# Optimization experiments

Measured on AMD Instinct MI355X. Metric: run time of the kernel, lower is better.

## Reference

```python
import jax, jax.numpy as jnp
import numpy as np

B, ND, NS, V, D, H, N, NL = 1024, 13, 26, 10000, 64, 8, 16, 4
SEQ = 1 + ND + NS  # cls + dense fields + sparse fields = 40


def _ln(x, g, b):
    m = x.mean(-1, keepdims=True)
    v = x.var(-1, keepdims=True)
    return (x - m) / jnp.sqrt(v + 1e-5) * g + b


def _mamba(x, g, b, xW, xb, A, Dp, oW, ob):
    # Faithful to MambaBlock: normed x feeds proj, state, and D-skip; residual is pre-norm x.
    xn = _ln(x, g, b)
    xp = xn @ xW.T + xb                              # (B,L,2D)
    delta, Bm = jnp.split(xp, 2, axis=-1)
    delta = jax.nn.softplus(delta)
    # h in torch is (B,L,D,1); (h*A_disc).sum(-1) == h * sum_n exp(delta*A[:,n])
    gate = jnp.exp(delta[..., None] * A).sum(-1)     # (B,L,D)
    h = jnp.cumsum(xn * Bm, axis=1)                  # (B,L,D)
    out = h * gate + xn * Dp
    return out @ oW.T + ob + x


def _fwd(dense_x, dense_W, dense_b, embed_tables, cls_token, mb_norm_g, mb_norm_b, mb_xproj_W, mb_xproj_b, mb_A, mb_D, mb_out_W, mb_out_b, merge_W, merge_b, attn_in_W, attn_in_b, attn_out_W, attn_out_b, mlp_W1, mlp_b1, mlp_W2, mlp_b2, mlp_W3, mlp_b3, sparse_idx):
    Bsz = dense_x.shape[0]
    dense_emb = (dense_x @ dense_W.T + dense_b).reshape(Bsz, ND, D)
    idx = jnp.clip(sparse_idx, 0, V)                 # clamp(0, num_embeddings-1)
    sparse_emb = embed_tables[jnp.arange(NS)[None, :], idx]   # (B,NS,D)
    seq = jnp.concatenate([jnp.broadcast_to(cls_token, (Bsz, 1, D)), dense_emb, sparse_emb], axis=1)
    for i in range(NL):
        f = _mamba(seq, mb_norm_g[i, 0], mb_norm_b[i, 0], mb_xproj_W[i, 0], mb_xproj_b[i, 0], mb_A[i, 0], mb_D[i, 0], mb_out_W[i, 0], mb_out_b[i, 0])
        r = _mamba(seq[:, ::-1], mb_norm_g[i, 1], mb_norm_b[i, 1], mb_xproj_W[i, 1], mb_xproj_b[i, 1], mb_A[i, 1], mb_D[i, 1], mb_out_W[i, 1], mb_out_b[i, 1])[:, ::-1]
        seq = jnp.concatenate([f, r], axis=-1) @ merge_W[i].T + merge_b[i]
    # nn.MultiheadAttention (batch_first, eval): packed qkv proj, scaled dot-product, out proj
    qkv = seq @ attn_in_W.T + attn_in_b
    q, k, v = jnp.split(qkv, 3, axis=-1)
    hd = D // H
    rs = lambda t: t.reshape(Bsz, SEQ, H, hd).transpose(0, 2, 1, 3)
    q, k, v = rs(q), rs(k), rs(v)
    att = jax.nn.softmax(jnp.einsum('bhqd,bhkd->bhqk', q, k) / float(np.sqrt(hd)), axis=-1)
    ao = jnp.einsum('bhqk,bhkd->bhqd', att, v).transpose(0, 2, 1, 3).reshape(Bsz, SEQ, D)
    seq = seq + ao @ attn_out_W.T + attn_out_b
    c = seq[:, 0]
    h1 = jax.nn.relu(c @ mlp_W1.T + mlp_b1)
    h2 = jax.nn.relu(h1 @ mlp_W2.T + mlp_b2)
    return (h2 @ mlp_W3.T + mlp_b3)[:, 0]


def setup_inputs():
    ks = iter(jax.random.split(jax.random.key(0), 64))
    nrm = lambda shape, s=0.02: jax.random.normal(next(ks), shape, jnp.float32) * s
    inp = {}
    inp['dense_x'] = jax.random.normal(next(ks), (B, ND), jnp.float32)
    inp['dense_W'] = nrm((ND * D, ND)); inp['dense_b'] = jnp.zeros((ND * D,), jnp.float32)
    tbl = nrm((NS, V + 1, D)); inp['embed_tables'] = tbl.at[:, 0, :].set(0.0)  # padding_idx=0
    inp['cls_token'] = nrm((1, 1, D))
    inp['mb_norm_g'] = jnp.ones((NL, 2, D), jnp.float32); inp['mb_norm_b'] = jnp.zeros((NL, 2, D), jnp.float32)
    inp['mb_xproj_W'] = nrm((NL, 2, 2 * D, D)); inp['mb_xproj_b'] = jnp.zeros((NL, 2, 2 * D), jnp.float32)
    inp['mb_A'] = jax.random.uniform(next(ks), (NL, 2, D, N), jnp.float32, -0.01, 0.01)
    inp['mb_D'] = jnp.ones((NL, 2, D), jnp.float32)
    inp['mb_out_W'] = nrm((NL, 2, D, D)); inp['mb_out_b'] = jnp.zeros((NL, 2, D), jnp.float32)
    inp['merge_W'] = nrm((NL, D, 2 * D)); inp['merge_b'] = jnp.zeros((NL, D), jnp.float32)
    inp['attn_in_W'] = nrm((3 * D, D)); inp['attn_in_b'] = jnp.zeros((3 * D,), jnp.float32)
    inp['attn_out_W'] = nrm((D, D)); inp['attn_out_b'] = jnp.zeros((D,), jnp.float32)
    inp['mlp_W1'] = nrm((128, D)); inp['mlp_b1'] = jnp.zeros((128,), jnp.float32)
    inp['mlp_W2'] = nrm((64, 128)); inp['mlp_b2'] = jnp.zeros((64,), jnp.float32)
    inp['mlp_W3'] = nrm((1, 64)); inp['mlp_b3'] = jnp.zeros((1,), jnp.float32)
    inp['sparse_x'] = jax.random.randint(next(ks), (B, NS), 0, V, jnp.int32)
    return inp


def reference(dense_x, dense_W, dense_b, embed_tables, cls_token, mb_norm_g, mb_norm_b, mb_xproj_W, mb_xproj_b, mb_A, mb_D, mb_out_W, mb_out_b, merge_W, merge_b, attn_in_W, attn_in_b, attn_out_W, attn_out_b, mlp_W1, mlp_b1, mlp_W2, mlp_b2, mlp_W3, mlp_b3, sparse_x):
    return _fwd(dense_x, dense_W, dense_b, embed_tables, cls_token, mb_norm_g, mb_norm_b, mb_xproj_W, mb_xproj_b, mb_A, mb_D, mb_out_W, mb_out_b, merge_W, merge_b, attn_in_W, attn_in_b, attn_out_W, attn_out_b, mlp_W1, mlp_b1, mlp_W2, mlp_b2, mlp_W3, mlp_b3, sparse_x)
```

## Files before the change

kernel.cpp:

```cpp
#include <hip/hip_runtime.h>

#define DEV static __device__ __forceinline__

typedef __attribute__((ext_vector_type(8))) short bf16x8;
typedef __attribute__((ext_vector_type(4))) float f32x4;

#define MFMA(a, b, c) __builtin_amdgcn_mfma_f32_16x16x32_bf16(a, b, c, 0, 0, 0)

DEV float bf2f(unsigned short h) { return __uint_as_float(((unsigned)h) << 16); }
DEV unsigned short f2bf(float f) {
  unsigned u = __float_as_uint(f);
  u += 0x7fffu + ((u >> 16) & 1u);
  return (unsigned short)(u >> 16);
}
DEV bf16x8 ld8(const unsigned short* p) { return *(const bf16x8*)p; }

DEV float dotg64(const float* x, const float* wrow) {
  const float4* wp = (const float4*)wrow;
  float a0 = 0.f, a1 = 0.f;
  #pragma unroll
  for (int c = 0; c < 8; ++c) {
    float4 u = wp[2*c], v = wp[2*c + 1];
    a0 = fmaf(u.x, x[8*c+0], a0); a0 = fmaf(u.y, x[8*c+1], a0);
    a0 = fmaf(u.z, x[8*c+2], a0); a0 = fmaf(u.w, x[8*c+3], a0);
    a1 = fmaf(v.x, x[8*c+4], a1); a1 = fmaf(v.y, x[8*c+5], a1);
    a1 = fmaf(v.z, x[8*c+6], a1); a1 = fmaf(v.w, x[8*c+7], a1);
  }
  return a0 + a1;
}
DEV float wred64(float v) {
  #pragma unroll
  for (int o = 32; o > 0; o >>= 1) v += __shfl_xor(v, o, 64);
  return v;
}

#define XW_HI 0
#define XW_LO 65536
#define OW_HI 131072
#define OW_LO 163840
#define MW_HI 196608
#define MW_LO 229376
#define AI_HI 262144
#define AI_LO 274432
#define SC_OFF 286720


__global__ void prep_kernel(const float* __restrict__ xW, const float* __restrict__ oW,
                            const float* __restrict__ mW, const float* __restrict__ aiW,
                            const float* __restrict__ Ap, unsigned short* __restrict__ wsb) {
  const int gid = blockIdx.x * blockDim.x + threadIdx.x;
  const int stride = gridDim.x * blockDim.x;
  for (int i = gid; i < 65536; i += stride) {
    float x = xW[i]; unsigned short h = f2bf(x);
    wsb[XW_HI + i] = h; wsb[XW_LO + i] = f2bf(x - bf2f(h));
  }
  for (int i = gid; i < 32768; i += stride) {
    float x = oW[i]; unsigned short h = f2bf(x);
    wsb[OW_HI + i] = h; wsb[OW_LO + i] = f2bf(x - bf2f(h));
  }
  for (int i = gid; i < 32768; i += stride) {
    float x = mW[i]; unsigned short h = f2bf(x);
    wsb[MW_HI + i] = h; wsb[MW_LO + i] = f2bf(x - bf2f(h));
  }
  for (int i = gid; i < 12288; i += stride) {
    float x = aiW[i]; unsigned short h = f2bf(x);
    wsb[AI_HI + i] = h; wsb[AI_LO + i] = f2bf(x - bf2f(h));
  }
  float* sc = (float*)(wsb + SC_OFF);
  for (int i = gid; i < 512; i += stride) {
    int pi = i >> 6, d = i & 63;
    const float* a = Ap + (size_t)i * 16;
    float s1 = 0, s2 = 0, s3 = 0, s4 = 0;
    #pragma unroll
    for (int n = 0; n < 16; ++n) {
      float z = a[n]; float z2 = z * z;
      s1 += z; s2 += z2; s3 += z2 * z; s4 += z2 * z2;
    }
    sc[pi*256 + d]       = s1;
    sc[pi*256 + 64 + d]  = s2 * 0.5f;
    sc[pi*256 + 128 + d] = s3 * (1.f/6.f);
    sc[pi*256 + 192 + d] = s4 * (1.f/24.f);
  }
}

__global__ __launch_bounds__(512, 2)
void Mamba4CTRV9_kernel(
    const float* __restrict__ dense_x, const float* __restrict__ dense_W,
    const float* __restrict__ dense_b, const float* __restrict__ tbl,
    const float* __restrict__ cls, const float* __restrict__ ng,
    const float* __restrict__ nb, const float* __restrict__ xb,
    const float* __restrict__ Dp, const float* __restrict__ ob,
    const float* __restrict__ mb, const float* __restrict__ aib,
    const float* __restrict__ aoW, const float* __restrict__ aob,
    const float* __restrict__ w1, const float* __restrict__ b1,
    const float* __restrict__ w2, const float* __restrict__ b2,
    const float* __restrict__ w3, const float* __restrict__ b3,
    const int* __restrict__ sidx, const unsigned short* __restrict__ wsb,
    float* __restrict__ out) {
  __shared__ __align__(16) unsigned char smem[145408];
  float*          s_seq  = (float*)smem;
  unsigned short* s_xnb  = (unsigned short*)(smem + 40960);
  unsigned short* bG0    = (unsigned short*)(smem + 61440);
  unsigned short* bG1    = (unsigned short*)(smem + 81920);
  unsigned short* bB0    = (unsigned short*)(smem + 102400);
  unsigned short* bB1    = (unsigned short*)(smem + 122880);
  float*          s_small= (float*)(smem + 143360);
  float* g0f = (float*)bG0;
  float* g1f = (float*)bG1;
  const float* scf = (const float*)(wsb + SC_OFF);

  const int tid = threadIdx.x, b = blockIdx.x;
  const int lane = tid & 63, wv = tid >> 6;
  const int arow = lane & 15;
  const int aq = (lane >> 4) * 8;
  const int rq = (lane >> 4) * 4;
  const int rq7 = rq & 7;
  const int swA = (arow & 7) << 3;
  const int aqs0 = aq ^ swA, aqs1 = (aq + 32) ^ swA;

  {
    float* s_dx = s_small;
    int* s_idx = (int*)(s_small + 64);
    if (tid < 64) {
      int br = tid >> 4, k = tid & 15;
      if (k < 13) s_dx[tid] = dense_x[(b*4 + br)*13 + k];
    }
    if (tid >= 64 && tid < 168) {
      int s = tid - 64, br = s / 26, si = s - br*26;
      int v = sidx[(b*4 + br)*26 + si];
      v = v < 0 ? 0 : (v > 10000 ? 10000 : v);
      s_idx[s] = v;
    }
    __syncthreads();
    if (tid < 256) s_seq[(tid >> 6)*40*64 + (tid & 63)] = cls[tid & 63];
    {
      const int br = tid >> 7, j0 = tid & 127;
      float x[13];
      #pragma unroll
      for (int k = 0; k < 13; ++k) x[k] = s_dx[br*16 + k];
      for (int j = j0; j < 832; j += 128) {
        float acc = dense_b[j];
        #pragma unroll
        for (int k = 0; k < 13; ++k) acc = fmaf(x[k], dense_W[j*13 + k], acc);
        s_seq[(br*40 + 1 + (j >> 6))*64 + (j & 63)] = acc;
      }
    }
    for (int e = tid; e < 1664; e += 512) {
      int br = e / 416, rem = e - br*416, s = rem >> 4, c = rem & 15;
      const float4* row = (const float4*)(tbl + ((size_t)(s*10001 + s_idx[br*26 + s]))*64);
      ((float4*)&s_seq[(br*40 + 14 + s)*64])[c] = row[c];
    }
  }
  __syncthreads();

  for (int L = 0; L < 4; ++L) {
    const int pi0 = 2*L, pi1 = 2*L + 1;

    {
      const int half = lane >> 5, dl = lane & 31;
      const float ng0 = ng[pi0*64 + dl], ng1 = ng[pi0*64 + dl + 32];
      const float nb0 = nb[pi0*64 + dl], nb1 = nb[pi0*64 + dl + 32];
      #pragma unroll 1
      for (int it = 0; it < 10; ++it) {
        int t = wv*20 + it*2 + half;
        int e = t*64 + dl;
        float x0 = s_seq[e], x1 = s_seq[e + 32];
        float s = x0 + x1, q = fmaf(x0, x0, x1*x1);
        #pragma unroll
        for (int o = 16; o > 0; o >>= 1) { s += __shfl_xor(s, o, 64); q += __shfl_xor(q, o, 64); }
        float mean = s * (1.f/64.f);
        float var = q * (1.f/64.f) - mean*mean;
        float rs = rsqrtf(var + 1e-5f);
        float xn0 = fmaf((x0 - mean) * rs, ng0, nb0);
        float xn1 = fmaf((x1 - mean) * rs, ng1, nb1);
        int sw = (t & 7) << 3;
        int eb = t << 6;
        s_xnb[eb + (dl ^ sw)] = f2bf(xn0);
        s_xnb[eb + ((dl + 32) ^ sw)] = f2bf(xn1);
      }
    }
    __syncthreads();

    {
      const int j = wv*16 + arow;
      const unsigned short* Wh0 = wsb + XW_HI + pi0*8192 + j*64;
      const unsigned short* Wl0 = wsb + XW_LO + pi0*8192 + j*64;
      const unsigned short* Wh1 = wsb + XW_HI + pi1*8192 + j*64;
      const unsigned short* Wl1 = wsb + XW_LO + pi1*8192 + j*64;
      bf16x8 bh00 = ld8(Wh0 + aq), bh01 = ld8(Wh0 + 32 + aq);
      bf16x8 bl00 = ld8(Wl0 + aq), bl01 = ld8(Wl0 + 32 + aq);
      bf16x8 bh10 = ld8(Wh1 + aq), bh11 = ld8(Wh1 + 32 + aq);
      bf16x8 bl10 = ld8(Wl1 + aq), bl11 = ld8(Wl1 + 32 + aq);
      const float bj0 = xb[pi0*128 + j], bj1 = xb[pi1*128 + j];
      const bool isDelta = (wv < 4);
      float c10=0,c20=0,c30=0,c40=0,c11=0,c21=0,c31=0,c41=0;
      if (isDelta) {
        c10=scf[pi0*256+j]; c20=scf[pi0*256+64+j]; c30=scf[pi0*256+128+j]; c40=scf[pi0*256+192+j];
        c11=scf[pi1*256+j]; c21=scf[pi1*256+64+j]; c31=scf[pi1*256+128+j]; c41=scf[pi1*256+192+j];
      }
      #pragma unroll 1
      for (int mt = 0; mt < 10; ++mt) {
        const unsigned short* A = s_xnb + ((mt*16 + arow) << 6);
        bf16x8 ah0 = ld8(A + aqs0), ah1 = ld8(A + aqs1);
        f32x4 a0 = {0,0,0,0}, a1 = {0,0,0,0};
        a0 = MFMA(ah0, bh00, a0); a0 = MFMA(ah0, bl00, a0);
        a0 = MFMA(ah1, bh01, a0); a0 = MFMA(ah1, bl01, a0);
        a1 = MFMA(ah0, bh10, a1); a1 = MFMA(ah0, bl10, a1);
        a1 = MFMA(ah1, bh11, a1); a1 = MFMA(ah1, bl11, a1);
        const int rbase = mt*16 + rq;
        #pragma unroll
        for (int r = 0; r < 4; ++r) {
          int row = rbase + r;
          int swr = (rq7 + r) << 3;
          float x0v = a0[r] + bj0, x1v = a1[r] + bj1;
          if (isDelta) {
            float sp0 = fmaxf(x0v, 0.f) + __logf(1.f + __expf(-fabsf(x0v)));
            float sp1 = fmaxf(x1v, 0.f) + __logf(1.f + __expf(-fabsf(x1v)));
            int o = (row << 6) + (j ^ swr);
            bG0[o] = f2bf(sp0 * fmaf(sp0, fmaf(sp0, fmaf(sp0, c40, c30), c20), c10));
            bG1[o] = f2bf(sp1 * fmaf(sp1, fmaf(sp1, fmaf(sp1, c41, c31), c21), c11));
          } else {
            int o = (row << 6) + ((j - 64) ^ swr);
            bB0[o] = f2bf(x0v);
            bB1[o] = f2bf(x1v);
          }
        }
      }
    }
    __syncthreads();

    {
      const int d = tid & 63, dir = (tid >> 6) & 1, br = tid >> 7;
      const unsigned short* bmb = dir ? bB1 : bB0;
      unsigned short* gb = dir ? bG1 : bG0;
      const float dpd = Dp[(pi0 + dir)*64 + d];
      const int base = br*40;
      float run = 0.f;
      #pragma unroll
      for (int k = 0; k < 40; ++k) {
        int t = base + (dir ? (39 - k) : k);
        int o = (t << 6) + (d ^ ((t & 7) << 3));
        float xn = bf2f(s_xnb[o]);
        run = fmaf(xn, bf2f(bmb[o]), run);
        float gate = 16.f + bf2f(gb[o]);
        gb[o] = f2bf(fmaf(run, gate, xn * dpd));
      }
    }
    __syncthreads();

    {
      const int j = (wv & 3)*16 + arow;
      const int mt0 = (wv < 4) ? 0 : 5, mt1 = (wv < 4) ? 5 : 10;
      const unsigned short* Wh0 = wsb + OW_HI + pi0*4096 + j*64;
      const unsigned short* Wl0 = wsb + OW_LO + pi0*4096 + j*64;
      const unsigned short* Wh1 = wsb + OW_HI + pi1*4096 + j*64;
      const unsigned short* Wl1 = wsb + OW_LO + pi1*4096 + j*64;
      bf16x8 bh00 = ld8(Wh0 + aq), bh01 = ld8(Wh0 + 32 + aq);
      bf16x8 bl00 = ld8(Wl0 + aq), bl01 = ld8(Wl0 + 32 + aq);
      bf16x8 bh10 = ld8(Wh1 + aq), bh11 = ld8(Wh1 + 32 + aq);
      bf16x8 bl10 = ld8(Wl1 + aq), bl11 = ld8(Wl1 + 32 + aq);
      const float bo0 = ob[pi0*64 + j], bo1 = ob[pi1*64 + j];
      #pragma unroll 1
      for (int mt = mt0; mt < mt1; ++mt) {
        const unsigned short* A0 = bG0 + ((mt*16 + arow) << 6);
        const unsigned short* A1 = bG1 + ((mt*16 + arow) << 6);
        bf16x8 a00 = ld8(A0 + aqs0), a01 = ld8(A0 + aqs1);
        bf16x8 a10 = ld8(A1 + aqs0), a11 = ld8(A1 + aqs1);
        f32x4 c0 = {0,0,0,0}, c1 = {0,0,0,0};
        c0 = MFMA(a00, bh00, c0); c0 = MFMA(a00, bl00, c0);
        c0 = MFMA(a01, bh01, c0); c0 = MFMA(a01, bl01, c0);
        c1 = MFMA(a10, bh10, c1); c1 = MFMA(a10, bl10, c1);
        c1 = MFMA(a11, bh11, c1); c1 = MFMA(a11, bl11, c1);
        const int rbase = mt*16 + rq;
        #pragma unroll
        for (int r = 0; r < 4; ++r) {
          int row = rbase + r;
          int o = (row << 6) + (j ^ ((rq7 + r) << 3));
          float res = s_seq[row*64 + j];
          bB0[o] = f2bf(c0[r] + bo0 + res);
          bB1[o] = f2bf(c1[r] + bo1 + res);
        }
      }
    }
    __syncthreads();

    {
      const int n0 = (wv & 3)*16 + arow;
      const int mt0 = (wv < 4) ? 0 : 5, mt1 = (wv < 4) ? 5 : 10;
      const unsigned short* Wh = wsb + MW_HI + L*8192 + n0*128;
      const unsigned short* Wl = wsb + MW_LO + L*8192 + n0*128;
      bf16x8 bh[4], bl[4];
      #pragma unroll
      for (int ks = 0; ks < 4; ++ks) { bh[ks] = ld8(Wh + ks*32 + aq); bl[ks] = ld8(Wl + ks*32 + aq); }
      const float bo = mb[L*64 + n0];
      #pragma unroll 1
      for (int mt = mt0; mt < mt1; ++mt) {
        const unsigned short* Af = bB0 + ((mt*16 + arow) << 6);
        const unsigned short* Ar = bB1 + ((mt*16 + arow) << 6);
        bf16x8 fh0 = ld8(Af + aqs0), fh1 = ld8(Af + aqs1);
        bf16x8 rh0 = ld8(Ar + aqs0), rh1 = ld8(Ar + aqs1);
        f32x4 a0 = {0,0,0,0};
        a0 = MFMA(fh0, bh[0], a0); a0 = MFMA(fh0, bl[0], a0);
        a0 = MFMA(fh1, bh[1], a0); a0 = MFMA(fh1, bl[1], a0);
        a0 = MFMA(rh0, bh[2], a0); a0 = MFMA(rh0, bl[2], a0);
        a0 = MFMA(rh1, bh[3], a0); a0 = MFMA(rh1, bl[3], a0);
        const int rbase = mt*16 + rq;
        #pragma unroll
        for (int r = 0; r < 4; ++r) {
          int row = rbase + r;
          float v = a0[r] + bo;
          s_seq[row*64 + n0] = v;
          if (L == 3) s_xnb[(row << 6) + (n0 ^ ((rq7 + r) << 3))] = f2bf(v);
        }
      }
    }
    __syncthreads();
  }

  {
    #pragma unroll 1
    for (int i = 0; i < 12; ++i) {
      const int u = wv + 8*i;
      int j, mtk;
      if (u < 80) { j = 64 + (u & 7)*16 + arow; mtk = u >> 3; }
      else {
        int qi = u - 80;
        j = (qi & 3)*16 + arow;
        int p = qi >> 2;
        mtk = p*2 + (p >> 1);
      }
      const unsigned short* Wh = wsb + AI_HI + j*64;
      const unsigned short* Wl = wsb + AI_LO + j*64;
      bf16x8 bh0 = ld8(Wh + aq), bh1 = ld8(Wh + 32 + aq);
      bf16x8 bl0 = ld8(Wl + aq), bl1 = ld8(Wl + 32 + aq);
      const float bj = aib[j];
      const unsigned short* A = s_xnb + ((mtk*16 + arow) << 6);
      bf16x8 ah0 = ld8(A + aqs0), ah1 = ld8(A + aqs1);
      f32x4 a0 = {0,0,0,0};
      a0 = MFMA(ah0, bh0, a0); a0 = MFMA(ah0, bl0, a0);
      a0 = MFMA(ah1, bh1, a0); a0 = MFMA(ah1, bl1, a0);
      const int rbase = mtk*16 + rq;
      #pragma unroll
      for (int r = 0; r < 4; ++r) {
        int row = rbase + r;
        int swr = (rq7 + r) << 3;
        float val = a0[r] + bj;
        if (u < 80) {
          if (j < 128) bB0[(row << 6) + ((j - 64) ^ swr)] = f2bf(val);
          else         bB1[(row << 6) + ((j - 128) ^ swr)] = f2bf(val);
        } else {
          if (row % 40 == 0) g0f[(row/40)*720 + 320 + j] = val;
        }
      }
    }
    if (tid < 256) g0f[(tid >> 6)*720 + 384 + (tid & 63)] = s_seq[(tid >> 6)*40*64 + (tid & 63)];
  }
  __syncthreads();

  for (int e = tid; e < 1280; e += 512) {
    int br = e / 320, rem = e - br*320;
    int h = rem / 40, kk = rem - h*40;
    int row = br*40 + kk;
    int kbase = (row << 6) + ((h*8) ^ ((kk & 7) << 3));
    float acc = 0.f;
    #pragma unroll
    for (int i = 0; i < 8; ++i)
      acc += g0f[br*720 + 320 + h*8 + i] * bf2f(bB0[kbase + i]);
    g0f[br*720 + rem] = acc * 0.35355339059327373f;
  }
  __syncthreads();

  {
    const int hh = wv*4 + (lane >> 4), jl = lane & 15;
    float* pr = g0f + (hh >> 3)*720 + (hh & 7)*40;
    float a = pr[jl];
    float bv = pr[16 + jl];
    float cv = (jl < 8) ? pr[32 + jl] : -1e30f;
    float m = fmaxf(fmaxf(a, bv), cv);
    #pragma unroll
    for (int o = 8; o > 0; o >>= 1) m = fmaxf(m, __shfl_xor(m, o, 16));
    float pa = __expf(a - m), pb = __expf(bv - m), pc = (jl < 8) ? __expf(cv - m) : 0.f;
    float s = pa + pb + pc;
    #pragma unroll
    for (int o = 8; o > 0; o >>= 1) s += __shfl_xor(s, o, 16);
    float inv = 1.f / s;
    pr[jl] = pa * inv;
    pr[16 + jl] = pb * inv;
    if (jl < 8) pr[32 + jl] = pc * inv;
  }
  __syncthreads();

  for (int e = tid; e < 1024; e += 512) {
    const int d = e & 63, qrt = (e >> 6) & 3, br = e >> 8, hh = d >> 3;
    float acc = 0.f;
    #pragma unroll
    for (int k = qrt*10; k < qrt*10 + 10; ++k) {
      int o = ((br*40 + k) << 6) + (d ^ ((k & 7) << 3));
      acc += g0f[br*720 + hh*40 + k] * bf2f(bB1[o]);
    }
    g1f[br*512 + qrt*64 + d] = acc;
  }
  __syncthreads();
  if (tid < 256) {
    float* p = g1f + (tid >> 6)*512;
    int d = tid & 63;
    p[256 + d] = p[d] + p[64 + d] + p[128 + d] + p[192 + d];
  }
  __syncthreads();

  if (tid < 256) {
    int br = tid >> 6, o = tid & 63;
    g0f[br*720 + 448 + o] = g0f[br*720 + 384 + o] + aob[o]
                          + dotg64(&g1f[br*512 + 256], aoW + (size_t)o*64);
  }
  __syncthreads();

  {
    int br = tid >> 7, o = tid & 127;
    g1f[br*512 + 320 + o] = fmaxf(b1[o] + dotg64(&g0f[br*720 + 448], w1 + (size_t)o*64), 0.f);
  }
  __syncthreads();

  if (tid < 256) {
    int br = tid >> 6, o = tid & 63;
    float acc = dotg64(&g1f[br*512 + 320], w2 + (size_t)o*128)
              + dotg64(&g1f[br*512 + 384], w2 + (size_t)o*128 + 64);
    g1f[br*512 + 448 + o] = fmaxf(acc + b2[o], 0.f);
  }
  __syncthreads();

  if (tid < 256) {
    int br = tid >> 6;
    float v = g1f[br*512 + 448 + lane] * w3[lane];
    v = wred64(v);
    if (lane == 0) out[b*4 + br] = v + b3[0];
  }
}

extern "C" void kernel_launch(void* const* d_in, const int* in_sizes, int n_in,
                              void* d_out, int out_size, void* d_ws, size_t ws_size,
                              hipStream_t stream) {
  (void)n_in; (void)ws_size; (void)out_size;
  const float* dense_x = (const float*)d_in[0];
  const float* dense_W = (const float*)d_in[1];
  const float* dense_b = (const float*)d_in[2];
  const float* tbl     = (const float*)d_in[3];
  const float* cls     = (const float*)d_in[4];
  const float* ng      = (const float*)d_in[5];
  const float* nb      = (const float*)d_in[6];
  const float* xW      = (const float*)d_in[7];
  const float* xb      = (const float*)d_in[8];
  const float* Ap      = (const float*)d_in[9];
  const float* Dp      = (const float*)d_in[10];
  const float* oW      = (const float*)d_in[11];
  const float* ob      = (const float*)d_in[12];
  const float* mW      = (const float*)d_in[13];
  const float* mb      = (const float*)d_in[14];
  const float* aiW     = (const float*)d_in[15];
  const float* aib     = (const float*)d_in[16];
  const float* aoW     = (const float*)d_in[17];
  const float* aob     = (const float*)d_in[18];
  const float* w1      = (const float*)d_in[19];
  const float* b1      = (const float*)d_in[20];
  const float* w2      = (const float*)d_in[21];
  const float* b2      = (const float*)d_in[22];
  const float* w3      = (const float*)d_in[23];
  const float* b3      = (const float*)d_in[24];
  const int*   sidx    = (const int*)d_in[25];
  float* out = (float*)d_out;
  unsigned short* wsb = (unsigned short*)d_ws;

  hipLaunchKernelGGL(prep_kernel, dim3(256), dim3(256), 0, stream,
                     xW, oW, mW, aiW, Ap, wsb);

  const int B = in_sizes[0] / 13;
  hipLaunchKernelGGL(Mamba4CTRV9_kernel, dim3(B/4), dim3(512), 0, stream,
                     dense_x, dense_W, dense_b, tbl, cls, ng, nb, xb, Dp, ob, mb,
                     aib, aoW, aob, w1, b1, w2, b2, w3, b3, sidx, wsb, out);
}
```

Before: 251.4 us.

## Fold Mamba out-projection into merge projection via precomputed combined weights

The per-layer out-projection and merge GEMMs are algebraically combined. The prep kernel precomputes merge_W·out_W for each direction, the summed residual weight, and a fused bias. The main kernel then runs one GEMM stage over the two gated outputs plus the residual, which removes one stage, one barrier and one bf16 round-trip through shared memory per layer. The scan loop also stages the residual into bf16 for this purpose. In exchange the prep kernel does more work, and the product weights and bf16-quantized residual may shift numerics slightly.

```diff
diff --git a/kernel.cpp b/kernel.cpp
--- a/kernel.cpp
+++ b/kernel.cpp
@@ -36,17 +36,16 @@
 
 #define XW_HI 0
 #define XW_LO 65536
-#define OW_HI 131072
-#define OW_LO 163840
-#define MW_HI 196608
-#define MW_LO 229376
+#define CW 131072
 #define AI_HI 262144
 #define AI_LO 274432
 #define SC_OFF 286720
+#define BP_OFF 290816
 
 
 __global__ void prep_kernel(const float* __restrict__ xW, const float* __restrict__ oW,
-                            const float* __restrict__ mW, const float* __restrict__ aiW,
+                            const float* __restrict__ ob, const float* __restrict__ mW,
+                            const float* __restrict__ mb, const float* __restrict__ aiW,
                             const float* __restrict__ Ap, unsigned short* __restrict__ wsb) {
   const int gid = blockIdx.x * blockDim.x + threadIdx.x;
   const int stride = gridDim.x * blockDim.x;
@@ -55,12 +54,38 @@
     wsb[XW_HI + i] = h; wsb[XW_LO + i] = f2bf(x - bf2f(h));
   }
   for (int i = gid; i < 32768; i += stride) {
-    float x = oW[i]; unsigned short h = f2bf(x);
-    wsb[OW_HI + i] = h; wsb[OW_LO + i] = f2bf(x - bf2f(h));
-  }
-  for (int i = gid; i < 32768; i += stride) {
-    float x = mW[i]; unsigned short h = f2bf(x);
-    wsb[MW_HI + i] = h; wsb[MW_LO + i] = f2bf(x - bf2f(h));
+    int L = i >> 13, rem = i & 8191;
+    int dir = rem >> 12, n = (rem >> 6) & 63, d = rem & 63;
+    const float* mrow = mW + L*8192 + n*128 + dir*64;
+    const float* ocol = oW + L*8192 + dir*4096 + d;
+    float acc = 0.f;
+    #pragma unroll 8
+    for (int j = 0; j < 64; ++j) acc = fmaf(mrow[j], ocol[j*64], acc);
+    unsigned short h = f2bf(acc);
+    int base = CW + L*24576 + dir*8192;
+    wsb[base + n*64 + d] = h;
+    wsb[base + 4096 + n*64 + d] = f2bf(acc - bf2f(h));
+  }
+  for (int i = gid; i < 16384; i += stride) {
+    int L = i >> 12, n = (i >> 6) & 63, j = i & 63;
+    float v = mW[L*8192 + n*128 + j] + mW[L*8192 + n*128 + 64 + j];
+    unsigned short h = f2bf(v);
+    int base = CW + L*24576 + 16384;
+    wsb[base + n*64 + j] = h;
+    wsb[base + 4096 + n*64 + j] = f2bf(v - bf2f(h));
+  }
+  {
+    float* bp = (float*)(wsb + BP_OFF);
+    for (int i = gid; i < 256; i += stride) {
+      int L = i >> 6, n = i & 63;
+      const float* mrow = mW + L*8192 + n*128;
+      float acc = mb[L*64 + n];
+      #pragma unroll 8
+      for (int j = 0; j < 64; ++j) acc = fmaf(ob[(2*L)*64 + j], mrow[j], acc);
+      #pragma unroll 8
+      for (int j = 0; j < 64; ++j) acc = fmaf(ob[(2*L+1)*64 + j], mrow[64 + j], acc);
+      bp[i] = acc;
+    }
   }
   for (int i = gid; i < 12288; i += stride) {
     float x = aiW[i]; unsigned short h = f2bf(x);
@@ -84,7 +109,7 @@
 }
 
 __global__ __launch_bounds__(512, 2)
-void Mamba4CTRV9_kernel(
+void Mamba4CTRV12_kernel(
     const float* __restrict__ dense_x, const float* __restrict__ dense_W,
     const float* __restrict__ dense_b, const float* __restrict__ tbl,
     const float* __restrict__ cls, const float* __restrict__ ng,
@@ -108,6 +133,7 @@
   float* g0f = (float*)bG0;
   float* g1f = (float*)bG1;
   const float* scf = (const float*)(wsb + SC_OFF);
+  const float* bpf = (const float*)(wsb + BP_OFF);
 
   const int tid = threadIdx.x, b = blockIdx.x;
   const int lane = tid & 63, wv = tid >> 6;
@@ -231,7 +257,7 @@
 
     {
       const int d = tid & 63, dir = (tid >> 6) & 1, br = tid >> 7;
-      const unsigned short* bmb = dir ? bB1 : bB0;
+      unsigned short* bmb = dir ? bB1 : bB0;
       unsigned short* gb = dir ? bG1 : bG0;
       const float dpd = Dp[(pi0 + dir)*64 + d];
       const int base = br*40;
@@ -244,71 +270,48 @@
         run = fmaf(xn, bf2f(bmb[o]), run);
         float gate = 16.f + bf2f(gb[o]);
         gb[o] = f2bf(fmaf(run, gate, xn * dpd));
+        if (dir == 0) bmb[o] = f2bf(s_seq[t*64 + d]);
       }
     }
     __syncthreads();
 
     {
-      const int j = (wv & 3)*16 + arow;
+      const int n0 = (wv & 3)*16 + arow;
       const int mt0 = (wv < 4) ? 0 : 5, mt1 = (wv < 4) ? 5 : 10;
-      const unsigned short* Wh0 = wsb + OW_HI + pi0*4096 + j*64;
-      const unsigned short* Wl0 = wsb + OW_LO + pi0*4096 + j*64;
-      const unsigned short* Wh1 = wsb + OW_HI + pi1*4096 + j*64;
-      const unsigned short* Wl1 = wsb + OW_LO + pi1*4096 + j*64;
-      bf16x8 bh00 = ld8(Wh0 + aq), bh01 = ld8(Wh0 + 32 + aq);
-      bf16x8 bl00 = ld8(Wl0 + aq), bl01 = ld8(Wl0 + 32 + aq);
-      bf16x8 bh10 = ld8(Wh1 + aq), bh11 = ld8(Wh1 + 32 + aq);
-      bf16x8 bl10 = ld8(Wl1 + aq), bl11 = ld8(Wl1 + 32 + aq);
-      const float bo0 = ob[pi0*64 + j], bo1 = ob[pi1*64 + j];
+      const unsigned short* cbase = wsb + CW + L*24576;
+      const unsigned short* C0H = cbase + n0*64;
+      const unsigned short* C0L = cbase + 4096 + n0*64;
+      const unsigned short* C1H = cbase + 8192 + n0*64;
+      const unsigned short* C1L = cbase + 12288 + n0*64;
+      const unsigned short* SH  = cbase + 16384 + n0*64;
+      const unsigned short* SL  = cbase + 20480 + n0*64;
+      bf16x8 c0h0 = ld8(C0H + aq), c0h1 = ld8(C0H + 32 + aq);
+      bf16x8 c0l0 = ld8(C0L + aq), c0l1 = ld8(C0L + 32 + aq);
+      bf16x8 c1h0 = ld8(C1H + aq), c1h1 = ld8(C1H + 32 + aq);
+      bf16x8 c1l0 = ld8(C1L + aq), c1l1 = ld8(C1L + 32 + aq);
+      bf16x8 sh0 = ld8(SH + aq), sh1 = ld8(SH + 32 + aq);
+      bf16x8 sl0 = ld8(SL + aq), sl1 = ld8(SL + 32 + aq);
+      const float bom = bpf[L*64 + n0];
       #pragma unroll 1
       for (int mt = mt0; mt < mt1; ++mt) {
         const unsigned short* A0 = bG0 + ((mt*16 + arow) << 6);
         const unsigned short* A1 = bG1 + ((mt*16 + arow) << 6);
-        bf16x8 a00 = ld8(A0 + aqs0), a01 = ld8(A0 + aqs1);
-        bf16x8 a10 = ld8(A1 + aqs0), a11 = ld8(A1 + aqs1);
-        f32x4 c0 = {0,0,0,0}, c1 = {0,0,0,0};
-        c0 = MFMA(a00, bh00, c0); c0 = MFMA(a00, bl00, c0);
-        c0 = MFMA(a01, bh01, c0); c0 = MFMA(a01, bl01, c0);
-        c1 = MFMA(a10, bh10, c1); c1 = MFMA(a10, bl10, c1);
-        c1 = MFMA(a11, bh11, c1); c1 = MFMA(a11, bl11, c1);
+        const unsigned short* AR = bB0 + ((mt*16 + arow) << 6);
+        bf16x8 g00 = ld8(A0 + aqs0), g01 = ld8(A0 + aqs1);
+        bf16x8 g10 = ld8(A1 + aqs0), g11 = ld8(A1 + aqs1);
+        bf16x8 r0 = ld8(AR + aqs0), r1 = ld8(AR + aqs1);
+        f32x4 a0 = {0,0,0,0}, a1 = {0,0,0,0}, a2 = {0,0,0,0};
+        a0 = MFMA(g00, c0h0, a0); a0 = MFMA(g00, c0l0, a0);
+        a0 = MFMA(g01, c0h1, a0); a0 = MFMA(g01, c0l1, a0);
+        a1 = MFMA(g10, c1h0, a1); a1 = MFMA(g10, c1l0, a1);
+        a1 = MFMA(g11, c1h1, a1); a1 = MFMA(g11, c1l1, a1);
+        a2 = MFMA(r0, sh0, a2); a2 = MFMA(r0, sl0, a2);
+        a2 = MFMA(r1, sh1, a2); a2 = MFMA(r1, sl1, a2);
         const int rbase = mt*16 + rq;
         #pragma unroll
         for (int r = 0; r < 4; ++r) {
           int row = rbase + r;
-          int o = (row << 6) + (j ^ ((rq7 + r) << 3));
-          float res = s_seq[row*64 + j];
-          bB0[o] = f2bf(c0[r] + bo0 + res);
-          bB1[o] = f2bf(c1[r] + bo1 + res);
-        }
-      }
-    }
-    __syncthreads();
-
-    {
-      const int n0 = (wv & 3)*16 + arow;
-      const int mt0 = (wv < 4) ? 0 : 5, mt1 = (wv < 4) ? 5 : 10;
-      const unsigned short* Wh = wsb + MW_HI + L*8192 + n0*128;
-      const unsigned short* Wl = wsb + MW_LO + L*8192 + n0*128;
-      bf16x8 bh[4], bl[4];
-      #pragma unroll
-      for (int ks = 0; ks < 4; ++ks) { bh[ks] = ld8(Wh + ks*32 + aq); bl[ks] = ld8(Wl + ks*32 + aq); }
-      const float bo = mb[L*64 + n0];
-      #pragma unroll 1
-      for (int mt = mt0; mt < mt1; ++mt) {
-        const unsigned short* Af = bB0 + ((mt*16 + arow) << 6);
-        const unsigned short* Ar = bB1 + ((mt*16 + arow) << 6);
-        bf16x8 fh0 = ld8(Af + aqs0), fh1 = ld8(Af + aqs1);
-        bf16x8 rh0 = ld8(Ar + aqs0), rh1 = ld8(Ar + aqs1);
-        f32x4 a0 = {0,0,0,0};
-        a0 = MFMA(fh0, bh[0], a0); a0 = MFMA(fh0, bl[0], a0);
-        a0 = MFMA(fh1, bh[1], a0); a0 = MFMA(fh1, bl[1], a0);
-        a0 = MFMA(rh0, bh[2], a0); a0 = MFMA(rh0, bl[2], a0);
-        a0 = MFMA(rh1, bh[3], a0); a0 = MFMA(rh1, bl[3], a0);
-        const int rbase = mt*16 + rq;
-        #pragma unroll
-        for (int r = 0; r < 4; ++r) {
-          int row = rbase + r;
-          float v = a0[r] + bo;
+          float v = a0[r] + a1[r] + a2[r] + bom;
           s_seq[row*64 + n0] = v;
           if (L == 3) s_xnb[(row << 6) + (n0 ^ ((rq7 + r) << 3))] = f2bf(v);
         }
@@ -471,10 +474,10 @@
   unsigned short* wsb = (unsigned short*)d_ws;
 
   hipLaunchKernelGGL(prep_kernel, dim3(256), dim3(256), 0, stream,
-                     xW, oW, mW, aiW, Ap, wsb);
+                     xW, oW, ob, mW, mb, aiW, Ap, wsb);
 
   const int B = in_sizes[0] / 13;
-  hipLaunchKernelGGL(Mamba4CTRV9_kernel, dim3(B/4), dim3(512), 0, stream,
+  hipLaunchKernelGGL(Mamba4CTRV12_kernel, dim3(B/4), dim3(512), 0, stream,
                      dense_x, dense_W, dense_b, tbl, cls, ng, nb, xb, Dp, ob, mb,
                      aib, aoW, aob, w1, b1, w2, b2, w3, b3, sidx, wsb, out);
 }
```

Result: slower. 256.5 us (+2.0%).
